# Kernel tuning notes

Measured on AMD Instinct MI355X. Metric: run time of the kernel, lower is better.

The kernel has to match this reference:

```python
import jax, jax.numpy as jnp
import numpy as np

B, S, E, F, N = 2, 1024, 1024, 2048, 8


def setup_inputs() -> dict:
    key = jax.random.key(0)
    k0, k1, k2, k3, k4 = jax.random.split(key, 5)
    x = jax.random.normal(k0, (B, S, E), dtype=jnp.float32)
    # fan_in-scaled params, matching nd_dense_init(1.0, 'fan_in', ...)
    gate_kernel = jax.random.normal(k1, (E, N), dtype=jnp.float32) / np.sqrt(E).astype(np.float32)
    w0 = jax.random.normal(k2, (N, E, F), dtype=jnp.float32) / np.sqrt(E).astype(np.float32)
    w1 = jax.random.normal(k3, (N, E, F), dtype=jnp.float32) / np.sqrt(E).astype(np.float32)
    wo = jax.random.normal(k4, (N, F, E), dtype=jnp.float32) / np.sqrt(F).astype(np.float32)
    return {"x": x, "gate_kernel": gate_kernel, "w0": w0, "w1": w1, "wo": wo, "top_k": 2}


def reference(x, gate_kernel, w0, w1, wo, top_k):
    # x: [B, S, E] -> tokens [T, E]
    b, s, e = x.shape
    n = gate_kernel.shape[-1]
    xf = x.reshape(b * s, e)
    # Router: gate logits + top-k expert selection, softmax over top-k (fp32, as in permute())
    logits = jnp.einsum('te,en->tn', xf, gate_kernel)
    top_w, top_e = jax.lax.top_k(logits, top_k)               # [T, K]
    probs = jax.nn.softmax(top_w.astype(jnp.float32), axis=-1)  # [T, K]
    # Combine weights per (token, expert): scatter top-k probs into [T, N]
    combine = jnp.einsum('tk,tkn->tn', probs, jax.nn.one_hot(top_e, n, dtype=jnp.float32))
    # Expert FFN (dropless): h = silu(x@w0) * (x@w1); out_e = h @ wo   (same math as gmm path)
    h0 = jnp.einsum('te,nef->ntf', xf, w0)                    # [N, T, F]
    h1 = jnp.einsum('te,nef->ntf', xf, w1)
    h = jax.nn.silu(h0) * h1
    expert_out = jnp.einsum('ntf,nfe->nte', h, wo)            # [N, T, E]
    # Weighted combine over experts (matches unpermute's 'BKE,BK->BE' in fp32)
    out = jnp.einsum('nte,tn->te', expert_out, combine)
    return out.reshape(b, s, e)
```

## Files before the change

### kernel.cpp

```cpp
#include <hip/hip_runtime.h>
#include <hip/hip_bf16.h>

#define T_TOK 2048
#define E_DIM 1024
#define F_DIM 2048
#define N_EXP 8

typedef __attribute__((ext_vector_type(8))) short short8;
typedef __attribute__((ext_vector_type(4))) float f32x4;

#define SWZB(f) (((f) ^ ((f) >> 3)) & 7)

__device__ __forceinline__ short bf2s(__hip_bfloat16 v) {
  union { __hip_bfloat16 b; short s; } u; u.b = v; return u.s;
}

__device__ __forceinline__ void gload_lds16(const void* g, void* l) {
  __builtin_amdgcn_global_load_lds((const __attribute__((address_space(1))) void*)g,
                                   (__attribute__((address_space(3))) void*)l, 16, 0, 0);
}

__global__ __launch_bounds__(256) void convert_x_kernel(const float* __restrict__ x,
                                                        __hip_bfloat16* __restrict__ xb) {
  size_t i = ((size_t)blockIdx.x * 256 + threadIdx.x) * 8;
  float4 a = *(const float4*)(x + i);
  float4 b = *(const float4*)(x + i + 4);
  short8 o;
  o[0] = bf2s(__float2bfloat16(a.x)); o[1] = bf2s(__float2bfloat16(a.y));
  o[2] = bf2s(__float2bfloat16(a.z)); o[3] = bf2s(__float2bfloat16(a.w));
  o[4] = bf2s(__float2bfloat16(b.x)); o[5] = bf2s(__float2bfloat16(b.y));
  o[6] = bf2s(__float2bfloat16(b.z)); o[7] = bf2s(__float2bfloat16(b.w));
  *(short8*)(xb + i) = o;
}

__global__ __launch_bounds__(256) void router_kernel(const float* __restrict__ x,
                                                     const float* __restrict__ gk,
                                                     int* __restrict__ tk_e,
                                                     float* __restrict__ tk_p,
                                                     int* __restrict__ counts) {
  int w = threadIdx.x >> 6, l = threadIdx.x & 63;
  int t = blockIdx.x * 4 + w;
  const float* xr = x + (size_t)t * E_DIM;
  double acc[N_EXP];
#pragma unroll
  for (int n = 0; n < N_EXP; n++) acc[n] = 0.0;
  for (int j = 0; j < 16; j++) {
    int i = j * 64 + l;
    double xv = (double)xr[i];
    const float* g = gk + (size_t)i * N_EXP;
#pragma unroll
    for (int n = 0; n < N_EXP; n++) acc[n] += xv * (double)g[n];
  }
#pragma unroll
  for (int off = 32; off > 0; off >>= 1) {
#pragma unroll
    for (int n = 0; n < N_EXP; n++) acc[n] += __shfl_down(acc[n], off);
  }
  if (l == 0) {
    int e1 = 0; double v1 = acc[0];
    for (int n = 1; n < N_EXP; n++) if (acc[n] > v1) { v1 = acc[n]; e1 = n; }
    int e2 = -1; double v2 = -1e300;
    for (int n = 0; n < N_EXP; n++) if (n != e1 && acc[n] > v2) { v2 = acc[n]; e2 = n; }
    float ex = __expf((float)(v2 - v1));
    float p1 = 1.f / (1.f + ex);
    float p2 = ex / (1.f + ex);
    tk_e[t * 2 + 0] = e1; tk_p[t * 2 + 0] = p1;
    tk_e[t * 2 + 1] = e2; tk_p[t * 2 + 1] = p2;
    atomicAdd(&counts[e1], 1);
    atomicAdd(&counts[e2], 1);
  }
}

__global__ __launch_bounds__(256) void scanperm_kernel(const int* __restrict__ tk_e,
                                                       const float* __restrict__ tk_p,
                                                       int* __restrict__ ctrl,
                                                       int* __restrict__ slot_tok,
                                                       float* __restrict__ slot_prob,
                                                       int* __restrict__ inv) {
  __shared__ int offs[8], cur[8];
  int tid = threadIdx.x;
  if (tid == 0) {
    int off = 0, idx = 0;
    for (int e = 0; e < N_EXP; e++) {
      offs[e] = off; cur[e] = 0;
      int c = ctrl[e];
      for (int m0 = 0; m0 < c; m0 += 128) {
        ctrl[32 + idx] = e;
        ctrl[96 + idx] = off + m0;
        ctrl[160 + idx] = (c - m0 < 128) ? (c - m0) : 128;
        idx++;
      }
      off += c;
    }
    ctrl[24] = idx;
  }
  __syncthreads();
  for (int g = tid; g < 2 * T_TOK; g += 256) {
    int e = tk_e[g];
    float p = tk_p[g];
    int pos = atomicAdd(&cur[e], 1);
    int slot = offs[e] + pos;
    slot_tok[slot] = g >> 1;
    slot_prob[slot] = p;
    inv[g] = slot;
  }
}

__global__ __launch_bounds__(512, 4) void gemm1_kernel(const __hip_bfloat16* __restrict__ xb,
                                                       const float* __restrict__ w0,
                                                       const float* __restrict__ w1,
                                                       const int* __restrict__ ctrl,
                                                       const int* __restrict__ slot_tok,
                                                       __hip_bfloat16* __restrict__ h) {
  int lin = blockIdx.x;
  int logical = (lin & 7) * 80 + (lin >> 3);
  int mt = logical % 40;
  int fy = logical / 40;
  if (mt >= ctrl[24]) return;
  int e = ctrl[32 + mt];
  int slot0 = ctrl[96 + mt];
  int rowsv = ctrl[160 + mt];
  int f0 = fy * 128;

  __shared__ alignas(16) short lA[128 * 64];
  __shared__ alignas(16) short lB0[128 * 64];
  __shared__ alignas(16) short lB1[128 * 64];

  int tid = threadIdx.x;
  int w = tid >> 6, l = tid & 63;
  int wm = w >> 2, wn = w & 3;
  int frow = l & 15, fk = l >> 4;

  int r1 = tid >> 3;
  int kcA = ((tid & 7) ^ (r1 & 7)) * 8;
  int tokA1 = slot_tok[slot0 + r1];
  int tokA2 = slot_tok[slot0 + r1 + 64];
  const __hip_bfloat16* aS1 = xb + (size_t)tokA1 * E_DIM + kcA;
  const __hip_bfloat16* aS2 = xb + (size_t)tokA2 * E_DIM + kcA;

  int uf = tid & 31, uk = tid >> 5;
  const float* b0s = w0 + ((size_t)e * E_DIM + uk * 4) * F_DIM + f0 + uf * 4;
  const float* b1s = w1 + ((size_t)e * E_DIM + uk * 4) * F_DIM + f0 + uf * 4;
  int elB[4];
#pragma unroll
  for (int j = 0; j < 4; ++j) {
    int f = uf * 4 + j;
    elB[j] = f * 64 + (((uk >> 1) ^ SWZB(f)) & 7) * 8 + (uk & 1) * 4;
  }

  f32x4 zero4 = {0.f, 0.f, 0.f, 0.f};
  f32x4 acc0[4][2], acc1[4][2];
#pragma unroll
  for (int mi = 0; mi < 4; mi++)
#pragma unroll
    for (int ni = 0; ni < 2; ni++) { acc0[mi][ni] = zero4; acc1[mi][ni] = zero4; }

  const int NT = E_DIM / 64;
  for (int t = 0; t < NT; ++t) {
    if (t) __syncthreads();
    int k0 = t * 64;
    gload_lds16(aS1 + k0, &lA[w * 512]);
    gload_lds16(aS2 + k0, &lA[4096 + w * 512]);
    {
      float4 r[4];
#pragma unroll
      for (int rr = 0; rr < 4; ++rr)
        r[rr] = *(const float4*)(b0s + (size_t)(k0 + rr) * F_DIM);
#pragma unroll
      for (int j = 0; j < 4; ++j) {
        short4 q;
        q.x = bf2s(__float2bfloat16(((const float*)&r[0])[j]));
        q.y = bf2s(__float2bfloat16(((const float*)&r[1])[j]));
        q.z = bf2s(__float2bfloat16(((const float*)&r[2])[j]));
        q.w = bf2s(__float2bfloat16(((const float*)&r[3])[j]));
        *(short4*)&lB0[elB[j]] = q;
      }
    }
    {
      float4 r[4];
#pragma unroll
      for (int rr = 0; rr < 4; ++rr)
        r[rr] = *(const float4*)(b1s + (size_t)(k0 + rr) * F_DIM);
#pragma unroll
      for (int j = 0; j < 4; ++j) {
        short4 q;
        q.x = bf2s(__float2bfloat16(((const float*)&r[0])[j]));
        q.y = bf2s(__float2bfloat16(((const float*)&r[1])[j]));
        q.z = bf2s(__float2bfloat16(((const float*)&r[2])[j]));
        q.w = bf2s(__float2bfloat16(((const float*)&r[3])[j]));
        *(short4*)&lB1[elB[j]] = q;
      }
    }
    __syncthreads();
    __builtin_amdgcn_s_setprio(1);
#pragma unroll
    for (int ks = 0; ks < 2; ++ks) {
      short8 a[4], b0[2], b1[2];
#pragma unroll
      for (int mi = 0; mi < 4; ++mi) {
        int r = wm * 64 + mi * 16 + frow;
        a[mi] = *(const short8*)&lA[r * 64 + ((ks * 4 + fk) ^ (r & 7)) * 8];
      }
#pragma unroll
      for (int ni = 0; ni < 2; ++ni) {
        int n = wn * 32 + ni * 16 + frow;
        int off = n * 64 + (((ks * 4 + fk) ^ SWZB(n)) & 7) * 8;
        b0[ni] = *(const short8*)&lB0[off];
        b1[ni] = *(const short8*)&lB1[off];
      }
#pragma unroll
      for (int mi = 0; mi < 4; ++mi)
#pragma unroll
        for (int ni = 0; ni < 2; ++ni) {
          acc0[mi][ni] = __builtin_amdgcn_mfma_f32_16x16x32_bf16(a[mi], b0[ni], acc0[mi][ni], 0, 0, 0);
          acc1[mi][ni] = __builtin_amdgcn_mfma_f32_16x16x32_bf16(a[mi], b1[ni], acc1[mi][ni], 0, 0, 0);
        }
    }
    __builtin_amdgcn_s_setprio(0);
  }

#pragma unroll
  for (int mi = 0; mi < 4; ++mi) {
#pragma unroll
    for (int j = 0; j < 4; ++j) {
      int r = wm * 64 + mi * 16 + fk * 4 + j;
      if (r < rowsv) {
        __hip_bfloat16* hr = h + (size_t)(slot0 + r) * F_DIM + f0 + wn * 32;
#pragma unroll
        for (int ni = 0; ni < 2; ++ni) {
          float v0 = acc0[mi][ni][j];
          float v1 = acc1[mi][ni][j];
          float s = (v0 / (1.f + __expf(-v0))) * v1;
          hr[ni * 16 + frow] = __float2bfloat16(s);
        }
      }
    }
  }
}

__global__ __launch_bounds__(512, 4) void gemm2_kernel(const __hip_bfloat16* __restrict__ h,
                                                       const float* __restrict__ wo,
                                                       const int* __restrict__ ctrl,
                                                       const float* __restrict__ slot_prob,
                                                       float* __restrict__ parts) {
  int lin = blockIdx.x;
  int logical = (lin & 7) * 40 + (lin >> 3);
  int mt = logical % 40;
  int ey = logical / 40;
  if (mt >= ctrl[24]) return;
  int e = ctrl[32 + mt];
  int slot0 = ctrl[96 + mt];
  int rowsv = ctrl[160 + mt];
  int e0 = ey * 128;

  __shared__ alignas(16) short lA[128 * 64];
  __shared__ alignas(16) short lB[128 * 64];

  int tid = threadIdx.x;
  int w = tid >> 6, l = tid & 63;
  int wm = w >> 2, wn = w & 3;
  int frow = l & 15, fk = l >> 4;

  int r1 = tid >> 3;
  int kcA = ((tid & 7) ^ (r1 & 7)) * 8;
  const __hip_bfloat16* aS1 = h + (size_t)(slot0 + r1) * F_DIM + kcA;
  const __hip_bfloat16* aS2 = aS1 + (size_t)64 * F_DIM;

  int ue = tid & 31, uk = tid >> 5;
  const float* bs = wo + ((size_t)e * F_DIM + uk * 4) * E_DIM + e0 + ue * 4;
  int elB[4];
#pragma unroll
  for (int j = 0; j < 4; ++j) {
    int f = ue * 4 + j;
    elB[j] = f * 64 + (((uk >> 1) ^ SWZB(f)) & 7) * 8 + (uk & 1) * 4;
  }

  f32x4 zero4 = {0.f, 0.f, 0.f, 0.f};
  f32x4 acc[4][2];
#pragma unroll
  for (int mi = 0; mi < 4; mi++)
#pragma unroll
    for (int ni = 0; ni < 2; ni++) acc[mi][ni] = zero4;

  const int NT = F_DIM / 64;
  for (int t = 0; t < NT; ++t) {
    if (t) __syncthreads();
    int k0 = t * 64;
    gload_lds16(aS1 + k0, &lA[w * 512]);
    gload_lds16(aS2 + k0, &lA[4096 + w * 512]);
    {
      float4 r[4];
#pragma unroll
      for (int rr = 0; rr < 4; ++rr)
        r[rr] = *(const float4*)(bs + (size_t)(k0 + rr) * E_DIM);
#pragma unroll
      for (int j = 0; j < 4; ++j) {
        short4 q;
        q.x = bf2s(__float2bfloat16(((const float*)&r[0])[j]));
        q.y = bf2s(__float2bfloat16(((const float*)&r[1])[j]));
        q.z = bf2s(__float2bfloat16(((const float*)&r[2])[j]));
        q.w = bf2s(__float2bfloat16(((const float*)&r[3])[j]));
        *(short4*)&lB[elB[j]] = q;
      }
    }
    __syncthreads();
    __builtin_amdgcn_s_setprio(1);
#pragma unroll
    for (int ks = 0; ks < 2; ++ks) {
      short8 a[4], b[2];
#pragma unroll
      for (int mi = 0; mi < 4; ++mi) {
        int r = wm * 64 + mi * 16 + frow;
        a[mi] = *(const short8*)&lA[r * 64 + ((ks * 4 + fk) ^ (r & 7)) * 8];
      }
#pragma unroll
      for (int ni = 0; ni < 2; ++ni) {
        int n = wn * 32 + ni * 16 + frow;
        b[ni] = *(const short8*)&lB[n * 64 + (((ks * 4 + fk) ^ SWZB(n)) & 7) * 8];
      }
#pragma unroll
      for (int mi = 0; mi < 4; ++mi)
#pragma unroll
        for (int ni = 0; ni < 2; ++ni)
          acc[mi][ni] = __builtin_amdgcn_mfma_f32_16x16x32_bf16(a[mi], b[ni], acc[mi][ni], 0, 0, 0);
    }
    __builtin_amdgcn_s_setprio(0);
  }

#pragma unroll
  for (int mi = 0; mi < 4; ++mi) {
#pragma unroll
    for (int j = 0; j < 4; ++j) {
      int r = wm * 64 + mi * 16 + fk * 4 + j;
      if (r < rowsv) {
        int slot = slot0 + r;
        float p = slot_prob[slot];
        float* pr = parts + (size_t)slot * E_DIM + e0 + wn * 32;
#pragma unroll
        for (int ni = 0; ni < 2; ++ni)
          pr[ni * 16 + frow] = p * acc[mi][ni][j];
      }
    }
  }
}

__global__ __launch_bounds__(256) void combine_kernel(const float* __restrict__ parts,
                                                      const int* __restrict__ inv,
                                                      float* __restrict__ out) {
  int g = blockIdx.x * 256 + threadIdx.x;
  int row = g >> 7, c = (g & 127) * 8;
  int s1 = inv[row * 2], s2 = inv[row * 2 + 1];
  const float4* p1 = (const float4*)(parts + (size_t)s1 * E_DIM + c);
  const float4* p2 = (const float4*)(parts + (size_t)s2 * E_DIM + c);
  float4 a0 = p1[0], a1 = p1[1], b0 = p2[0], b1 = p2[1];
  float4 o0 = {a0.x + b0.x, a0.y + b0.y, a0.z + b0.z, a0.w + b0.w};
  float4 o1 = {a1.x + b1.x, a1.y + b1.y, a1.z + b1.z, a1.w + b1.w};
  float4* op = (float4*)(out + (size_t)row * E_DIM + c);
  op[0] = o0; op[1] = o1;
}

extern "C" void kernel_launch(void* const* d_in, const int* in_sizes, int n_in,
                              void* d_out, int out_size, void* d_ws, size_t ws_size,
                              hipStream_t stream) {
  const float* x  = (const float*)d_in[0];
  const float* gk = (const float*)d_in[1];
  const float* w0 = (const float*)d_in[2];
  const float* w1 = (const float*)d_in[3];
  const float* wo = (const float*)d_in[4];
  float* out = (float*)d_out;
  char* ws = (char*)d_ws;

  const size_t SLOTS = 2 * T_TOK + 128;
  const size_t OFF_XB   = 0;
  const size_t OFF_H    = OFF_XB + (size_t)T_TOK * E_DIM * 2;
  const size_t OFF_PART = OFF_H + SLOTS * F_DIM * 2;
  const size_t OFF_STOK = OFF_PART + SLOTS * E_DIM * 4;
  const size_t OFF_SPRB = OFF_STOK + SLOTS * 4;
  const size_t OFF_TKE  = OFF_SPRB + SLOTS * 4;
  const size_t OFF_TKP  = OFF_TKE + (size_t)2 * T_TOK * 4;
  const size_t OFF_INV  = OFF_TKP + (size_t)2 * T_TOK * 4;
  const size_t OFF_CTRL = OFF_INV + (size_t)2 * T_TOK * 4;
  const size_t NEED     = OFF_CTRL + 1024;
  if (ws_size < NEED) return;

  __hip_bfloat16* xb   = (__hip_bfloat16*)(ws + OFF_XB);
  __hip_bfloat16* hbuf = (__hip_bfloat16*)(ws + OFF_H);
  float* parts     = (float*)(ws + OFF_PART);
  int*   slot_tok  = (int*)(ws + OFF_STOK);
  float* slot_prob = (float*)(ws + OFF_SPRB);
  int*   tk_e      = (int*)(ws + OFF_TKE);
  float* tk_p      = (float*)(ws + OFF_TKP);
  int*   inv       = (int*)(ws + OFF_INV);
  int*   ctrl      = (int*)(ws + OFF_CTRL);

  hipMemsetAsync(ctrl, 0, 1024, stream);
  hipMemsetAsync(slot_tok + 2 * T_TOK, 0, 128 * 4, stream);

  convert_x_kernel<<<(T_TOK * E_DIM) / (256 * 8), 256, 0, stream>>>(x, xb);
  router_kernel<<<T_TOK / 4, 256, 0, stream>>>(x, gk, tk_e, tk_p, ctrl);
  scanperm_kernel<<<1, 256, 0, stream>>>(tk_e, tk_p, ctrl, slot_tok, slot_prob, inv);
  gemm1_kernel<<<dim3(640), 512, 0, stream>>>(xb, w0, w1, ctrl, slot_tok, hbuf);
  gemm2_kernel<<<dim3(320), 512, 0, stream>>>(hbuf, wo, ctrl, slot_prob, parts);
  combine_kernel<<<(T_TOK * 128) / 256, 256, 0, stream>>>(parts, inv, out);
}
```

Baseline: 221.6 us.

## Prefetch fp32 expert weights into registers one K-tile ahead and rework LDS layout

Both expert GEMM kernels now issue global loads of the next K-tile of fp32 weights into registers right after the LDS barrier, so those loads overlap the MFMA work on the current tile. Each thread now loads 8 k-rows by 2 columns as float2 and writes them as 16-byte short8 stores into a new XOR-swizzled LDS layout, replacing the float4 loads and 8-byte short4 stores. The read-side swizzle is changed to match. The extra register buffers raise register pressure and may reduce occupancy, and float2 global loads are narrower than float4.

```diff
diff --git a/kernel.cpp b/kernel.cpp
--- a/kernel.cpp
+++ b/kernel.cpp
@@ -8,8 +8,6 @@
 
 typedef __attribute__((ext_vector_type(8))) short short8;
 typedef __attribute__((ext_vector_type(4))) float f32x4;
-
-#define SWZB(f) (((f) ^ ((f) >> 3)) & 7)
 
 __device__ __forceinline__ short bf2s(__hip_bfloat16 v) {
   union { __hip_bfloat16 b; short s; } u; u.b = v; return u.s;
@@ -138,15 +136,12 @@
   const __hip_bfloat16* aS1 = xb + (size_t)tokA1 * E_DIM + kcA;
   const __hip_bfloat16* aS2 = xb + (size_t)tokA2 * E_DIM + kcA;
 
-  int uf = tid & 31, uk = tid >> 5;
-  const float* b0s = w0 + ((size_t)e * E_DIM + uk * 4) * F_DIM + f0 + uf * 4;
-  const float* b1s = w1 + ((size_t)e * E_DIM + uk * 4) * F_DIM + f0 + uf * 4;
-  int elB[4];
-#pragma unroll
-  for (int j = 0; j < 4; ++j) {
-    int f = uf * 4 + j;
-    elB[j] = f * 64 + (((uk >> 1) ^ SWZB(f)) & 7) * 8 + (uk & 1) * 4;
-  }
+  int uf = tid & 63, uk = tid >> 6;
+  const float* b0s = w0 + ((size_t)e * E_DIM + uk * 8) * F_DIM + f0 + uf * 2;
+  const float* b1s = w1 + ((size_t)e * E_DIM + uk * 8) * F_DIM + f0 + uf * 2;
+  int elB = (uf * 2) * 64 + ((uk ^ (uf & 7)) * 8);
+
+  float2 rB0[8], rB1[8];
 
   f32x4 zero4 = {0.f, 0.f, 0.f, 0.f};
   f32x4 acc0[4][2], acc1[4][2];
@@ -155,43 +150,39 @@
 #pragma unroll
     for (int ni = 0; ni < 2; ni++) { acc0[mi][ni] = zero4; acc1[mi][ni] = zero4; }
 
+  auto loadB = [&](int t) {
+    const float* p0 = b0s + (size_t)t * 64 * F_DIM;
+    const float* p1 = b1s + (size_t)t * 64 * F_DIM;
+#pragma unroll
+    for (int rr = 0; rr < 8; ++rr) {
+      rB0[rr] = *(const float2*)(p0 + (size_t)rr * F_DIM);
+      rB1[rr] = *(const float2*)(p1 + (size_t)rr * F_DIM);
+    }
+  };
+  auto writeB = [&]() {
+#pragma unroll
+    for (int j = 0; j < 2; ++j) {
+      short8 q0, q1;
+#pragma unroll
+      for (int rr = 0; rr < 8; ++rr) {
+        q0[rr] = bf2s(__float2bfloat16(j ? rB0[rr].y : rB0[rr].x));
+        q1[rr] = bf2s(__float2bfloat16(j ? rB1[rr].y : rB1[rr].x));
+      }
+      *(short8*)&lB0[elB + j * 64] = q0;
+      *(short8*)&lB1[elB + j * 64] = q1;
+    }
+  };
+
+  loadB(0);
+
   const int NT = E_DIM / 64;
   for (int t = 0; t < NT; ++t) {
-    if (t) __syncthreads();
-    int k0 = t * 64;
-    gload_lds16(aS1 + k0, &lA[w * 512]);
-    gload_lds16(aS2 + k0, &lA[4096 + w * 512]);
-    {
-      float4 r[4];
-#pragma unroll
-      for (int rr = 0; rr < 4; ++rr)
-        r[rr] = *(const float4*)(b0s + (size_t)(k0 + rr) * F_DIM);
-#pragma unroll
-      for (int j = 0; j < 4; ++j) {
-        short4 q;
-        q.x = bf2s(__float2bfloat16(((const float*)&r[0])[j]));
-        q.y = bf2s(__float2bfloat16(((const float*)&r[1])[j]));
-        q.z = bf2s(__float2bfloat16(((const float*)&r[2])[j]));
-        q.w = bf2s(__float2bfloat16(((const float*)&r[3])[j]));
-        *(short4*)&lB0[elB[j]] = q;
-      }
-    }
-    {
-      float4 r[4];
-#pragma unroll
-      for (int rr = 0; rr < 4; ++rr)
-        r[rr] = *(const float4*)(b1s + (size_t)(k0 + rr) * F_DIM);
-#pragma unroll
-      for (int j = 0; j < 4; ++j) {
-        short4 q;
-        q.x = bf2s(__float2bfloat16(((const float*)&r[0])[j]));
-        q.y = bf2s(__float2bfloat16(((const float*)&r[1])[j]));
-        q.z = bf2s(__float2bfloat16(((const float*)&r[2])[j]));
-        q.w = bf2s(__float2bfloat16(((const float*)&r[3])[j]));
-        *(short4*)&lB1[elB[j]] = q;
-      }
-    }
     __syncthreads();
+    gload_lds16(aS1 + t * 64, &lA[w * 512]);
+    gload_lds16(aS2 + t * 64, &lA[4096 + w * 512]);
+    writeB();
+    __syncthreads();
+    if (t + 1 < NT) loadB(t + 1);
     __builtin_amdgcn_s_setprio(1);
 #pragma unroll
     for (int ks = 0; ks < 2; ++ks) {
@@ -204,7 +195,7 @@
 #pragma unroll
       for (int ni = 0; ni < 2; ++ni) {
         int n = wn * 32 + ni * 16 + frow;
-        int off = n * 64 + (((ks * 4 + fk) ^ SWZB(n)) & 7) * 8;
+        int off = n * 64 + (((ks * 4 + fk) ^ ((n >> 1) & 7))) * 8;
         b0[ni] = *(const short8*)&lB0[off];
         b1[ni] = *(const short8*)&lB1[off];
       }
@@ -266,14 +257,11 @@
   const __hip_bfloat16* aS1 = h + (size_t)(slot0 + r1) * F_DIM + kcA;
   const __hip_bfloat16* aS2 = aS1 + (size_t)64 * F_DIM;
 
-  int ue = tid & 31, uk = tid >> 5;
-  const float* bs = wo + ((size_t)e * F_DIM + uk * 4) * E_DIM + e0 + ue * 4;
-  int elB[4];
-#pragma unroll
-  for (int j = 0; j < 4; ++j) {
-    int f = ue * 4 + j;
-    elB[j] = f * 64 + (((uk >> 1) ^ SWZB(f)) & 7) * 8 + (uk & 1) * 4;
-  }
+  int ue = tid & 63, uk = tid >> 6;
+  const float* bs = wo + ((size_t)e * F_DIM + uk * 8) * E_DIM + e0 + ue * 2;
+  int elB = (ue * 2) * 64 + ((uk ^ (ue & 7)) * 8);
+
+  float2 rB[8];
 
   f32x4 zero4 = {0.f, 0.f, 0.f, 0.f};
   f32x4 acc[4][2];
@@ -282,28 +270,33 @@
 #pragma unroll
     for (int ni = 0; ni < 2; ni++) acc[mi][ni] = zero4;
 
+  auto loadB = [&](int t) {
+    const float* p = bs + (size_t)t * 64 * E_DIM;
+#pragma unroll
+    for (int rr = 0; rr < 8; ++rr)
+      rB[rr] = *(const float2*)(p + (size_t)rr * E_DIM);
+  };
+  auto writeB = [&]() {
+#pragma unroll
+    for (int j = 0; j < 2; ++j) {
+      short8 q;
+#pragma unroll
+      for (int rr = 0; rr < 8; ++rr)
+        q[rr] = bf2s(__float2bfloat16(j ? rB[rr].y : rB[rr].x));
+      *(short8*)&lB[elB + j * 64] = q;
+    }
+  };
+
+  loadB(0);
+
   const int NT = F_DIM / 64;
   for (int t = 0; t < NT; ++t) {
-    if (t) __syncthreads();
-    int k0 = t * 64;
-    gload_lds16(aS1 + k0, &lA[w * 512]);
-    gload_lds16(aS2 + k0, &lA[4096 + w * 512]);
-    {
-      float4 r[4];
-#pragma unroll
-      for (int rr = 0; rr < 4; ++rr)
-        r[rr] = *(const float4*)(bs + (size_t)(k0 + rr) * E_DIM);
-#pragma unroll
-      for (int j = 0; j < 4; ++j) {
-        short4 q;
-        q.x = bf2s(__float2bfloat16(((const float*)&r[0])[j]));
-        q.y = bf2s(__float2bfloat16(((const float*)&r[1])[j]));
-        q.z = bf2s(__float2bfloat16(((const float*)&r[2])[j]));
-        q.w = bf2s(__float2bfloat16(((const float*)&r[3])[j]));
-        *(short4*)&lB[elB[j]] = q;
-      }
-    }
     __syncthreads();
+    gload_lds16(aS1 + t * 64, &lA[w * 512]);
+    gload_lds16(aS2 + t * 64, &lA[4096 + w * 512]);
+    writeB();
+    __syncthreads();
+    if (t + 1 < NT) loadB(t + 1);
     __builtin_amdgcn_s_setprio(1);
 #pragma unroll
     for (int ks = 0; ks < 2; ++ks) {
@@ -316,7 +309,7 @@
 #pragma unroll
       for (int ni = 0; ni < 2; ++ni) {
         int n = wn * 32 + ni * 16 + frow;
-        b[ni] = *(const short8*)&lB[n * 64 + (((ks * 4 + fk) ^ SWZB(n)) & 7) * 8];
+        b[ni] = *(const short8*)&lB[n * 64 + (((ks * 4 + fk) ^ ((n >> 1) & 7))) * 8];
       }
 #pragma unroll
       for (int mi = 0; mi < 4; ++mi)
```

Measured after the change: 239.8 us. +8.2%, slower.
